# Optimization experiments

Hardware: AMD Instinct MI355X
Metric: run time of the kernel (lower is better)

Reference implementation:

```python
import jax, jax.numpy as jnp
import numpy as np

INV_SQRT2 = 0.7071067811865476
N, E, K, S = 10000, 120000, 8, 7
DE, DA, DT, DR, DC = 128, 128, 64, 16, 16
T = E * K

def act(x):
    return jax.nn.silu(x)

def residual_stack(x, Ws):
    # Ws: (n_layers, 2, D, D); GemNet ResidualLayer: two Dense+act, scaled skip
    for lw in Ws:
        y = act(act(x @ lw[0]) @ lw[1])
        x = (x + y) * INV_SQRT2
    return x

def bilinear(rbf_W1, sph, m, id_reduce, id_ragged, W):
    # EfficientInteractionBilinear (GemNet): ragged scatter into (E,Kmax,emb) then basis contractions
    m2 = jnp.zeros((rbf_W1.shape[0], sph.shape[1], m.shape[-1]), m.dtype)
    m2 = m2.at[id_reduce, id_ragged].set(m)          # (E, K, DT)
    sum_k = jnp.einsum('eks,ekc->esc', sph, m2)      # (E, S, DT)
    a = jnp.einsum('ejs,esc->ejc', rbf_W1, sum_k)    # (E, DC, DT)
    return jnp.einsum('ejc,cju->eu', a, W)           # (E, DT)

def _forward(h, m_st, rbf_h, rbf3, cbf_rbfW1, cbf_sph,
             W_mlp_st, W_m_kt, W_t_rbf, W_down, W_bil, W_st3, W_ts3,
             res_before, res_after, W_ae_rbf, W_ae_in, res_atom, W_asi, res_m,
             idx_s, idx_t, idx_swap, id3_kt, id3_st, id3_ragged_idx):
    x_skip = m_st @ W_mlp_st
    # --- TripletInteraction ---
    m_kt = act(m_st @ W_m_kt)
    m_kt = m_kt * (rbf3 @ W_t_rbf)        # scale_rbf == 1.0 (identity ScaleFactor)
    m_kt = act(m_kt @ W_down)             # (E, DT)
    xb = bilinear(cbf_rbfW1, cbf_sph, m_kt[id3_kt], id3_st, id3_ragged_idx, W_bil)
    x_st = act(xb @ W_st3)
    x_ts = act(xb @ W_ts3)[idx_swap]
    x3 = (x_st + x_ts) * INV_SQRT2
    # --- merge + residual stacks ---
    x = (x_skip + x3) * INV_SQRT2
    x = residual_stack(x, res_before)
    x = (x + m_st) * INV_SQRT2
    x = residual_stack(x, res_after)
    # --- AtomEmbedding: edge->atom scatter-add ---
    xa = x * (rbf_h @ W_ae_rbf)
    h2 = jax.ops.segment_sum(xa, idx_t, num_segments=h.shape[0])  # scale_sum == 1.0
    h_new = residual_stack(act(h2 @ W_ae_in), res_atom)
    # --- AtomSelfInteraction: gather-concat-Dense ---
    m = act(jnp.concatenate([h_new[idx_s], h_new[idx_t], x], axis=-1) @ W_asi)
    m = residual_stack(m, res_m)
    m = (m + x) * INV_SQRT2
    return h_new, m

def setup_inputs():
    key = jax.random.key(0)
    ks = jax.random.split(key, 24)
    def w(k, shape):
        return jax.random.normal(k, shape, jnp.float32) * (1.0 / np.sqrt(shape[-2]))
    return dict(
        h=jax.random.normal(ks[0], (N, DA), jnp.float32),
        m_st=jax.random.normal(ks[1], (E, DE), jnp.float32),
        rbf_h=jax.random.uniform(ks[2], (E, DR), jnp.float32),
        rbf3=jax.random.uniform(ks[3], (E, DR), jnp.float32),
        cbf_rbfW1=jax.random.normal(ks[4], (E, DC, S), jnp.float32) * 0.2,
        cbf_sph=jax.random.normal(ks[5], (E, K, S), jnp.float32) * 0.2,
        W_mlp_st=w(ks[6], (DE, DE)),
        W_m_kt=w(ks[7], (DE, DE)),
        W_t_rbf=w(ks[8], (DR, DE)),
        W_down=w(ks[9], (DE, DT)),
        W_bil=jax.random.normal(ks[10], (DT, DC, DT), jnp.float32) * (1.0 / np.sqrt(DT * DC)),
        W_st3=w(ks[11], (DT, DE)),
        W_ts3=w(ks[12], (DT, DE)),
        res_before=w(ks[13], (1, 2, DE, DE)),
        res_after=w(ks[14], (2, 2, DE, DE)),
        W_ae_rbf=w(ks[15], (DR, DE)),
        W_ae_in=w(ks[16], (DE, DA)),
        res_atom=w(ks[17], (2, 2, DA, DA)),
        W_asi=w(ks[18], (2 * DA + DE, DE)),
        res_m=w(ks[19], (2, 2, DE, DE)),
        idx_s=jax.random.randint(ks[20], (E,), 0, N, jnp.int32),
        idx_t=jax.random.randint(ks[21], (E,), 0, N, jnp.int32),
        idx_swap=jax.random.permutation(ks[22], E).astype(jnp.int32),
        id3_kt=jax.random.randint(ks[23], (T,), 0, E, jnp.int32),
        id3_st=jnp.repeat(jnp.arange(E, dtype=jnp.int32), K),
        id3_ragged_idx=jnp.tile(jnp.arange(K, dtype=jnp.int32), E),
    )

def reference(h, m_st, rbf_h, rbf3, cbf_rbfW1, cbf_sph,
              W_mlp_st, W_m_kt, W_t_rbf, W_down, W_bil, W_st3, W_ts3,
              res_before, res_after, W_ae_rbf, W_ae_in, res_atom, W_asi, res_m,
              idx_s, idx_t, idx_swap, id3_kt, id3_st, id3_ragged_idx):
    return _forward(h, m_st, rbf_h, rbf3, cbf_rbfW1, cbf_sph,
                    W_mlp_st, W_m_kt, W_t_rbf, W_down, W_bil, W_st3, W_ts3,
                    res_before, res_after, W_ae_rbf, W_ae_in, res_atom, W_asi, res_m,
                    idx_s, idx_t, idx_swap, id3_kt, id3_st, id3_ragged_idx)
```

## Files before the change

### kernel.cpp

```cpp
#include <hip/hip_runtime.h>


#define EE 120000
#define NA 10000

constexpr float C_INV = 0.70710678118654752440f;

using f32x4 = __attribute__((ext_vector_type(4))) float;
using f32x2 = __attribute__((ext_vector_type(2))) float;
using s16x8 = __attribute__((ext_vector_type(8))) short;
using s16x4 = __attribute__((ext_vector_type(4))) short;

__device__ __forceinline__ float act_silu(float x) { return x / (1.0f + __expf(-x)); }

__device__ __forceinline__ unsigned short f2bf(float f) {
    unsigned int u = __float_as_uint(f);
    u += 0x7fffu + ((u >> 16) & 1u);
    return (unsigned short)(u >> 16);
}
__device__ __forceinline__ float bf2f(unsigned short h) {
    return __uint_as_float(((unsigned int)h) << 16);
}
__device__ __forceinline__ unsigned int cvtpk(float a, float b) {
    unsigned int r;
    asm("v_cvt_pk_bf16_f32 %0, %1, %2" : "=v"(r) : "v"(a), "v"(b));
    return r;
}

template<int MT, int KQ>
__device__ __forceinline__ void load_w(const unsigned short* __restrict__ W, int KW,
                                       int l, s16x8 (&a)[MT][KQ])
{
    const int fr = l & 15;
    const int k8 = (l >> 4) << 3;
    #pragma unroll
    for (int mt = 0; mt < MT; ++mt)
        #pragma unroll
        for (int kq = 0; kq < KQ; ++kq)
            a[mt][kq] = *(const s16x8*)&W[(size_t)(mt * 16 + fr) * KW + kq * 32 + k8];
}

template<int MT, int NF, int KQ>
__device__ __forceinline__ void gemm_pre(
    const s16x8 (&a)[MT][KQ], const char* ldsB, int RS,
    int rowBase, int l, f32x4 (&acc)[MT][NF])
{
    const int fr = l & 15;
    const int k8 = (l >> 4) << 3;
    #pragma unroll
    for (int kq = 0; kq < KQ; ++kq) {
        s16x8 b[NF];
        #pragma unroll
        for (int nf = 0; nf < NF; ++nf) {
            const int row = rowBase + nf * 16 + fr;
            const int kb  = ((kq * 32 + k8) * 2) ^ ((row & 7) << 4);
            b[nf] = *(const s16x8*)(ldsB + row * RS + kb);
        }
        #pragma unroll
        for (int mt = 0; mt < MT; ++mt)
            #pragma unroll
            for (int nf = 0; nf < NF; ++nf)
                acc[mt][nf] = __builtin_amdgcn_mfma_f32_16x16x32_bf16(
                    a[mt][kq], b[nf], acc[mt][nf], 0, 0, 0);
    }
}

template<int MT, int NF>
__device__ __forceinline__ void zacc(f32x4 (&acc)[MT][NF])
{
    #pragma unroll
    for (int mt = 0; mt < MT; ++mt)
        #pragma unroll
        for (int nf = 0; nf < NF; ++nf)
            acc[mt][nf] = (f32x4){0.f, 0.f, 0.f, 0.f};
}

__device__ __forceinline__ void packA(char* lds, int RS, int row, int outF0, f32x4 v)
{
    uint2 p;
    p.x = cvtpk(v[0], v[1]);
    p.y = cvtpk(v[2], v[3]);
    *(uint2*)(lds + row * RS + ((outF0 * 2) ^ ((row & 7) << 4))) = p;
}

__device__ __forceinline__ void store_bf4(unsigned short* dst, f32x4 v)
{
    uint2 p;
    p.x = cvtpk(v[0], v[1]);
    p.y = cvtpk(v[2], v[3]);
    *(uint2*)dst = p;
}

template<int ROWS>
__device__ __forceinline__ void stage_f32(char* lds, const float* __restrict__ src,
                                          int row0, int M, int tid)
{
    #pragma unroll
    for (int u = 0; u < ROWS * 16 / 512; ++u) {
        const int flat = tid + u * 512;
        const int row  = flat >> 4;
        const int k8   = (flat & 15) << 3;
        const int grow = row0 + row;
        uint4 val = {0u, 0u, 0u, 0u};
        if (grow < M) {
            const float* p = src + (size_t)grow * 128 + k8;
            f32x4 lo = *(const f32x4*)p;
            f32x4 hi = *(const f32x4*)(p + 4);
            val.x = cvtpk(lo[0], lo[1]);
            val.y = cvtpk(lo[2], lo[3]);
            val.z = cvtpk(hi[0], hi[1]);
            val.w = cvtpk(hi[2], hi[3]);
        }
        *(uint4*)(lds + row * 256 + ((k8 * 2) ^ ((row & 7) << 4))) = val;
    }
}

template<bool MSTM, int NF>
__device__ __forceinline__ void res_layer(
    char* A, char* B,
    const unsigned short* W0, const unsigned short* W1,
    int wm, int wn, int l, f32x4 (&x)[2][NF],
    const s16x4 (*ms)[NF])
{
    const int fr = l & 15;
    const int fq = (l >> 4) << 2;

    s16x8 aw[2][4];
    load_w<2, 4>(W0 + (size_t)(wm * 32) * 128, 128, l, aw);
    f32x4 acc[2][NF];
    zacc(acc);
    gemm_pre<2, NF, 4>(aw, A, 256, wn * NF * 16, l, acc);

    s16x8 aw1[2][4];
    load_w<2, 4>(W1 + (size_t)(wm * 32) * 128, 128, l, aw1);

    #pragma unroll
    for (int mt = 0; mt < 2; ++mt)
        #pragma unroll
        for (int nf = 0; nf < NF; ++nf) {
            const int row = wn * NF * 16 + nf * 16 + fr;
            const int of0 = wm * 32 + mt * 16 + fq;
            f32x4 v;
            #pragma unroll
            for (int q = 0; q < 4; ++q) v[q] = act_silu(acc[mt][nf][q]);
            packA(B, 256, row, of0, v);
        }
    __syncthreads();

    zacc(acc);
    gemm_pre<2, NF, 4>(aw1, B, 256, wn * NF * 16, l, acc);
    #pragma unroll
    for (int mt = 0; mt < 2; ++mt)
        #pragma unroll
        for (int nf = 0; nf < NF; ++nf) {
            const int row = wn * NF * 16 + nf * 16 + fr;
            const int of0 = wm * 32 + mt * 16 + fq;
            #pragma unroll
            for (int q = 0; q < 4; ++q)
                x[mt][nf][q] = (x[mt][nf][q] + act_silu(acc[mt][nf][q])) * C_INV;
            if (MSTM) {
                #pragma unroll
                for (int q = 0; q < 4; ++q)
                    x[mt][nf][q] = (x[mt][nf][q] +
                                    bf2f((unsigned short)ms[mt][nf][q])) * C_INV;
            }
            packA(A, 256, row, of0, x[mt][nf]);
        }
    __syncthreads();
}

__device__ __forceinline__ s16x4 read_frag(const char* lds, int row, int of0)
{
    return *(const s16x4*)(lds + row * 256 + ((of0 * 2) ^ ((row & 7) << 4)));
}

__global__ __launch_bounds__(512, 4) void front_k(
    const float* __restrict__ m_st, const unsigned short* __restrict__ scale_b,
    const unsigned short* __restrict__ Wmkt, const unsigned short* __restrict__ Wdown,
    unsigned short* __restrict__ mkt_b)
{
    __shared__ char A[128 * 256];
    const int tid = threadIdx.x;
    const int l = tid & 63, w = tid >> 6, wm = w & 3, wn = w >> 2;
    const int fr = l & 15, fq = (l >> 4) << 2;
    const int row0 = blockIdx.x * 128;

    s16x8 aw[2][4];
    load_w<2, 4>(Wmkt + (size_t)(wm * 32) * 128, 128, l, aw);

    stage_f32<128>(A, m_st, row0, EE, tid);
    __syncthreads();

    f32x4 acc[2][4];
    zacc(acc);
    gemm_pre<2, 4, 4>(aw, A, 256, wn * 64, l, acc);

    s16x8 aw2[1][4];
    load_w<1, 4>(Wdown + (size_t)(wm * 16) * 128, 128, l, aw2);

    __syncthreads();
    #pragma unroll
    for (int mt = 0; mt < 2; ++mt)
        #pragma unroll
        for (int nf = 0; nf < 4; ++nf) {
            const int row = wn * 64 + nf * 16 + fr;
            const int grow = row0 + row;
            const int of0 = wm * 32 + mt * 16 + fq;
            f32x4 v = {0.f, 0.f, 0.f, 0.f};
            if (grow < EE) {
                s16x4 sc = *(const s16x4*)&scale_b[(size_t)grow * 128 + of0];
                #pragma unroll
                for (int q = 0; q < 4; ++q)
                    v[q] = act_silu(acc[mt][nf][q]) * bf2f((unsigned short)sc[q]);
            }
            packA(A, 256, row, of0, v);
        }
    __syncthreads();

    f32x4 acc2[1][4];
    zacc(acc2);
    gemm_pre<1, 4, 4>(aw2, A, 256, wn * 64, l, acc2);
    #pragma unroll
    for (int nf = 0; nf < 4; ++nf) {
        const int row = wn * 64 + nf * 16 + fr;
        const int grow = row0 + row;
        if (grow >= EE) continue;
        const int of0 = wm * 16 + fq;
        f32x4 v;
        #pragma unroll
        for (int q = 0; q < 4; ++q) v[q] = act_silu(acc2[0][nf][q]);
        store_bf4(&mkt_b[(size_t)grow * 64 + of0], v);
    }
}

__global__ __launch_bounds__(512, 4) void st3ts3_k(
    const unsigned short* __restrict__ xb_b,
    const unsigned short* __restrict__ Wst3, const unsigned short* __restrict__ Wts3,
    unsigned short* __restrict__ yst, unsigned short* __restrict__ yts)
{
    __shared__ char A[128 * 128];
    const int tid = threadIdx.x;
    const int l = tid & 63, w = tid >> 6, wm = w & 3, wn = w >> 2;
    const int fr = l & 15, fq = (l >> 4) << 2;
    const int row0 = blockIdx.x * 128;

    s16x8 awS[2][2], awT[2][2];
    load_w<2, 2>(Wst3 + (size_t)(wm * 32) * 64, 64, l, awS);
    load_w<2, 2>(Wts3 + (size_t)(wm * 32) * 64, 64, l, awT);

    #pragma unroll
    for (int u = 0; u < 2; ++u) {
        const int flat = tid + u * 512;
        const int row = flat >> 3;
        const int k8 = (flat & 7) << 3;
        const int grow = row0 + row;
        s16x8 v = {0, 0, 0, 0, 0, 0, 0, 0};
        if (grow < EE) v = *(const s16x8*)&xb_b[(size_t)grow * 64 + k8];
        *(s16x8*)(A + row * 128 + ((k8 * 2) ^ ((row & 7) << 4))) = v;
    }
    __syncthreads();

    f32x4 aS[2][4], aT[2][4];
    zacc(aS); zacc(aT);
    {
        const int k8 = (l >> 4) << 3;
        #pragma unroll
        for (int kq = 0; kq < 2; ++kq) {
            s16x8 b[4];
            #pragma unroll
            for (int nf = 0; nf < 4; ++nf) {
                const int row = wn * 64 + nf * 16 + fr;
                const int kb  = ((kq * 32 + k8) * 2) ^ ((row & 7) << 4);
                b[nf] = *(const s16x8*)(A + row * 128 + kb);
            }
            #pragma unroll
            for (int mt = 0; mt < 2; ++mt)
                #pragma unroll
                for (int nf = 0; nf < 4; ++nf) {
                    aS[mt][nf] = __builtin_amdgcn_mfma_f32_16x16x32_bf16(
                        awS[mt][kq], b[nf], aS[mt][nf], 0, 0, 0);
                    aT[mt][nf] = __builtin_amdgcn_mfma_f32_16x16x32_bf16(
                        awT[mt][kq], b[nf], aT[mt][nf], 0, 0, 0);
                }
        }
    }

    #pragma unroll
    for (int mt = 0; mt < 2; ++mt)
        #pragma unroll
        for (int nf = 0; nf < 4; ++nf) {
            const int row = wn * 64 + nf * 16 + fr;
            const int grow = row0 + row;
            if (grow >= EE) continue;
            const int of0 = wm * 32 + mt * 16 + fq;
            f32x4 vs, vt;
            #pragma unroll
            for (int q = 0; q < 4; ++q) {
                vs[q] = act_silu(aS[mt][nf][q]);
                vt[q] = act_silu(aT[mt][nf][q]);
            }
            store_bf4(&yst[(size_t)grow * 128 + of0], vs);
            store_bf4(&yts[(size_t)grow * 128 + of0], vt);
        }
}

__global__ __launch_bounds__(512, 4) void chain_k(
    const float* __restrict__ m_st,
    const unsigned short* __restrict__ yst, const unsigned short* __restrict__ yts,
    const int* __restrict__ idx_swap,
    const unsigned short* __restrict__ Wmlp,
    const unsigned short* __restrict__ Wrb0, const unsigned short* __restrict__ Wrb1,
    const unsigned short* __restrict__ Wra0, const unsigned short* __restrict__ Wra1,
    const unsigned short* __restrict__ Wra2, const unsigned short* __restrict__ Wra3,
    unsigned short* __restrict__ xb_out)
{
    __shared__ char A[128 * 256];
    __shared__ char B[128 * 256];
    const int tid = threadIdx.x;
    const int l = tid & 63, w = tid >> 6, wm = w & 3, wn = w >> 2;
    const int fr = l & 15, fq = (l >> 4) << 2;
    const int row0 = blockIdx.x * 128;

    s16x8 aw[2][4];
    load_w<2, 4>(Wmlp + (size_t)(wm * 32) * 128, 128, l, aw);

    stage_f32<128>(A, m_st, row0, EE, tid);
    __syncthreads();

    f32x4 acc[2][4];
    zacc(acc);
    gemm_pre<2, 4, 4>(aw, A, 256, wn * 64, l, acc);

    s16x4 ms[2][4];
    #pragma unroll
    for (int mt = 0; mt < 2; ++mt)
        #pragma unroll
        for (int nf = 0; nf < 4; ++nf)
            ms[mt][nf] = read_frag(A, wn * 64 + nf * 16 + fr, wm * 32 + mt * 16 + fq);

    f32x4 x[2][4];
    #pragma unroll
    for (int mt = 0; mt < 2; ++mt)
        #pragma unroll
        for (int nf = 0; nf < 4; ++nf) {
            const int row = wn * 64 + nf * 16 + fr;
            const int grow = row0 + row;
            const int of0 = wm * 32 + mt * 16 + fq;
            if (grow < EE) {
                s16x4 a = *(const s16x4*)&yst[(size_t)grow * 128 + of0];
                const int sw = idx_swap[grow];
                s16x4 b = *(const s16x4*)&yts[(size_t)sw * 128 + of0];
                #pragma unroll
                for (int q = 0; q < 4; ++q)
                    x[mt][nf][q] = (acc[mt][nf][q] +
                        (bf2f((unsigned short)a[q]) + bf2f((unsigned short)b[q])) * C_INV) * C_INV;
            } else {
                x[mt][nf] = (f32x4){0.f, 0.f, 0.f, 0.f};
            }
        }
    __syncthreads();
    #pragma unroll
    for (int mt = 0; mt < 2; ++mt)
        #pragma unroll
        for (int nf = 0; nf < 4; ++nf)
            packA(A, 256, wn * 64 + nf * 16 + fr, wm * 32 + mt * 16 + fq, x[mt][nf]);
    __syncthreads();

    res_layer<true , 4>(A, B, Wrb0, Wrb1, wm, wn, l, x, ms);
    res_layer<false, 4>(A, B, Wra0, Wra1, wm, wn, l, x, nullptr);
    res_layer<false, 4>(A, B, Wra2, Wra3, wm, wn, l, x, nullptr);

    #pragma unroll
    for (int mt = 0; mt < 2; ++mt)
        #pragma unroll
        for (int nf = 0; nf < 4; ++nf) {
            const int row = wn * 64 + nf * 16 + fr;
            const int grow = row0 + row;
            if (grow >= EE) continue;
            const int of0 = wm * 32 + mt * 16 + fq;
            store_bf4(&xb_out[(size_t)grow * 128 + of0], x[mt][nf]);
        }
}

__global__ __launch_bounds__(512, 4) void atom_k(
    const float* __restrict__ h2,
    const unsigned short* __restrict__ Wae,
    const unsigned short* __restrict__ Wr0, const unsigned short* __restrict__ Wr1,
    const unsigned short* __restrict__ Wr2, const unsigned short* __restrict__ Wr3,
    float* __restrict__ out_h, unsigned short* __restrict__ h_b)
{
    __shared__ char A[64 * 256];
    __shared__ char B[64 * 256];
    const int tid = threadIdx.x;
    const int l = tid & 63, w = tid >> 6, wm = w & 3, wn = w >> 2;
    const int fr = l & 15, fq = (l >> 4) << 2;
    const int row0 = blockIdx.x * 64;

    s16x8 aw[2][4];
    load_w<2, 4>(Wae + (size_t)(wm * 32) * 128, 128, l, aw);

    stage_f32<64>(A, h2, row0, NA, tid);
    __syncthreads();

    f32x4 acc[2][2];
    zacc(acc);
    gemm_pre<2, 2, 4>(aw, A, 256, wn * 32, l, acc);
    f32x4 x[2][2];
    #pragma unroll
    for (int mt = 0; mt < 2; ++mt)
        #pragma unroll
        for (int nf = 0; nf < 2; ++nf)
            #pragma unroll
            for (int q = 0; q < 4; ++q)
                x[mt][nf][q] = act_silu(acc[mt][nf][q]);
    __syncthreads();
    #pragma unroll
    for (int mt = 0; mt < 2; ++mt)
        #pragma unroll
        for (int nf = 0; nf < 2; ++nf)
            packA(A, 256, wn * 32 + nf * 16 + fr, wm * 32 + mt * 16 + fq, x[mt][nf]);
    __syncthreads();

    res_layer<false, 2>(A, B, Wr0, Wr1, wm, wn, l, x, nullptr);
    res_layer<false, 2>(A, B, Wr2, Wr3, wm, wn, l, x, nullptr);

    #pragma unroll
    for (int mt = 0; mt < 2; ++mt)
        #pragma unroll
        for (int nf = 0; nf < 2; ++nf) {
            const int row = wn * 32 + nf * 16 + fr;
            const int grow = row0 + row;
            if (grow >= NA) continue;
            const int of0 = wm * 32 + mt * 16 + fq;
            *(f32x4*)&out_h[(size_t)grow * 128 + of0] = x[mt][nf];
            store_bf4(&h_b[(size_t)grow * 128 + of0], x[mt][nf]);
        }
}

__global__ __launch_bounds__(512, 4) void asi_k(
    const unsigned short* __restrict__ h_b, const unsigned short* __restrict__ x_b,
    const int* __restrict__ idx_s, const int* __restrict__ idx_t,
    const unsigned short* __restrict__ Wasi,
    const unsigned short* __restrict__ Wm0, const unsigned short* __restrict__ Wm1,
    const unsigned short* __restrict__ Wm2, const unsigned short* __restrict__ Wm3,
    float* __restrict__ out_m)
{
    __shared__ char A[128 * 256];
    __shared__ char B[128 * 256];
    const int tid = threadIdx.x;
    const int l = tid & 63, w = tid >> 6, wm = w & 3, wn = w >> 2;
    const int fr = l & 15, fq = (l >> 4) << 2;
    const int row0 = blockIdx.x * 128;

    f32x4 acc[2][4];
    zacc(acc);

    for (int c = 0; c < 3; ++c) {
        s16x8 aw[2][4];
        load_w<2, 4>(Wasi + (size_t)(wm * 32) * 384 + c * 128, 384, l, aw);
        #pragma unroll
        for (int u = 0; u < 4; ++u) {
            const int flat = tid + u * 512;
            const int row = flat >> 4;
            const int k8 = (flat & 15) << 3;
            const int grow = row0 + row;
            s16x8 v = {0, 0, 0, 0, 0, 0, 0, 0};
            if (grow < EE) {
                const unsigned short* src =
                    (c == 0) ? h_b + (size_t)idx_s[grow] * 128
                  : (c == 1) ? h_b + (size_t)idx_t[grow] * 128
                             : x_b + (size_t)grow * 128;
                v = *(const s16x8*)&src[k8];
            }
            *(s16x8*)(A + row * 256 + ((k8 * 2) ^ ((row & 7) << 4))) = v;
        }
        __syncthreads();
        gemm_pre<2, 4, 4>(aw, A, 256, wn * 64, l, acc);
        __syncthreads();
    }

    f32x4 x[2][4];
    #pragma unroll
    for (int mt = 0; mt < 2; ++mt)
        #pragma unroll
        for (int nf = 0; nf < 4; ++nf)
            #pragma unroll
            for (int q = 0; q < 4; ++q)
                x[mt][nf][q] = act_silu(acc[mt][nf][q]);
    #pragma unroll
    for (int mt = 0; mt < 2; ++mt)
        #pragma unroll
        for (int nf = 0; nf < 4; ++nf)
            packA(A, 256, wn * 64 + nf * 16 + fr, wm * 32 + mt * 16 + fq, x[mt][nf]);
    __syncthreads();

    res_layer<false, 4>(A, B, Wm0, Wm1, wm, wn, l, x, nullptr);
    res_layer<false, 4>(A, B, Wm2, Wm3, wm, wn, l, x, nullptr);

    #pragma unroll
    for (int mt = 0; mt < 2; ++mt)
        #pragma unroll
        for (int nf = 0; nf < 4; ++nf) {
            const int row = wn * 64 + nf * 16 + fr;
            const int grow = row0 + row;
            if (grow >= EE) continue;
            const int of0 = wm * 32 + mt * 16 + fq;
            s16x4 xv = *(const s16x4*)&x_b[(size_t)grow * 128 + of0];
            f32x4 o;
            #pragma unroll
            for (int q = 0; q < 4; ++q)
                o[q] = (x[mt][nf][q] + bf2f((unsigned short)xv[q])) * C_INV;
            *(f32x4*)&out_m[(size_t)grow * 128 + of0] = o;
        }
}

__global__ __launch_bounds__(256) void rbf_scale_k(
    const float* __restrict__ A, const float* __restrict__ W,
    unsigned short* __restrict__ out, int M)
{
    __shared__ float Ws[16][128];
    const int tid = threadIdx.x;
    #pragma unroll
    for (int t = tid; t < 512; t += 256) {
        int kk = t >> 5, c4 = (t & 31) << 2;
        *(float4*)&Ws[kk][c4] = *(const float4*)(W + kk * 128 + c4);
    }
    __syncthreads();
    const int tx = tid & 31, ty = tid >> 5;
    const int row0 = blockIdx.x * 128;
    #pragma unroll
    for (int i = 0; i < 16; ++i) {
        const int row = row0 + ty + i * 8;
        if (row >= M) continue;
        float av[16];
        #pragma unroll
        for (int j = 0; j < 4; ++j) {
            float4 a = *(const float4*)(A + (size_t)row * 16 + j * 4);
            av[j * 4] = a.x; av[j * 4 + 1] = a.y; av[j * 4 + 2] = a.z; av[j * 4 + 3] = a.w;
        }
        f32x4 s = {0.f, 0.f, 0.f, 0.f};
        #pragma unroll
        for (int k = 0; k < 16; ++k) {
            float4 wv = *(const float4*)&Ws[k][tx * 4];
            s[0] += av[k] * wv.x; s[1] += av[k] * wv.y;
            s[2] += av[k] * wv.z; s[3] += av[k] * wv.w;
        }
        store_bf4(&out[(size_t)row * 128 + tx * 4], s);
    }
}

__global__ void hist_k(const int* __restrict__ idxt, int* __restrict__ cnt)
{
    int i = blockIdx.x * 256 + threadIdx.x;
    if (i < EE) atomicAdd(&cnt[idxt[i]], 1);
}

__global__ __launch_bounds__(256) void scan_k(const int* __restrict__ cnt,
                                              int* __restrict__ start, int* __restrict__ wrk)
{
    __shared__ int ps[256];
    const int t = threadIdx.x;
    int s = 0;
    for (int j = 0; j < 40; ++j) {
        int idx = t * 40 + j;
        if (idx < NA) s += cnt[idx];
    }
    ps[t] = s;
    __syncthreads();
    for (int off = 1; off < 256; off <<= 1) {
        int v = (t >= off) ? ps[t - off] : 0;
        __syncthreads();
        ps[t] += v;
        __syncthreads();
    }
    int run = ps[t] - s;
    for (int j = 0; j < 40; ++j) {
        int idx = t * 40 + j;
        if (idx < NA) {
            start[idx] = run;
            wrk[idx] = run;
            run += cnt[idx];
        }
    }
    if (t == 255) start[NA] = ps[255];
}

__global__ void place_k(const int* __restrict__ idxt, int* __restrict__ wrk,
                        int* __restrict__ order)
{
    int i = blockIdx.x * 256 + threadIdx.x;
    if (i < EE) {
        int pos = atomicAdd(&wrk[idxt[i]], 1);
        order[pos] = i;
    }
}

__global__ __launch_bounds__(256) void segsum_k(
    const unsigned short* __restrict__ x_b, const float* __restrict__ rbf_h,
    const float* __restrict__ Wae, const int* __restrict__ start,
    const int* __restrict__ order, float* __restrict__ h2)
{
    const int tid = threadIdx.x;
    const int l = tid & 63, w = tid >> 6;
    const int a = blockIdx.x * 4 + w;
    if (a >= NA) return;

    float wc[32];
    #pragma unroll
    for (int j = 0; j < 16; ++j) {
        f32x2 v = *(const f32x2*)(Wae + j * 128 + 2 * l);
        wc[2 * j] = v[0]; wc[2 * j + 1] = v[1];
    }

    const int s = start[a], e_end = start[a + 1];
    float acc0 = 0.f, acc1 = 0.f;
    for (int i = s; i < e_end; ++i) {
        const int e = __builtin_amdgcn_readfirstlane(order[i]);
        const unsigned int xv = *(const unsigned int*)(x_b + (size_t)e * 128 + 2 * l);
        const float* rp = rbf_h + (size_t)e * 16;
        float c0 = 0.f, c1 = 0.f;
        #pragma unroll
        for (int j = 0; j < 16; ++j) {
            float r = rp[j];
            c0 += r * wc[2 * j];
            c1 += r * wc[2 * j + 1];
        }
        acc0 += bf2f((unsigned short)(xv & 0xffff)) * c0;
        acc1 += bf2f((unsigned short)(xv >> 16)) * c1;
    }
    f32x2 o; o[0] = acc0; o[1] = acc1;
    *(f32x2*)&h2[(size_t)a * 128 + 2 * l] = o;
}

__global__ void wconv_k(const float* __restrict__ Wbil, unsigned short* __restrict__ WT)
{
    int t = blockIdx.x * 256 + threadIdx.x;
    int u = t >> 10, k = t & 1023, j = k >> 6, c = k & 63;
    WT[t] = f2bf(Wbil[(size_t)(c * 16 + j) * 64 + u]);
}

struct WDesc { const float* src; int K; int N; int off; };
struct WTab  { WDesc d[21]; };

__global__ void wconvall_k(WTab tab, unsigned short* __restrict__ dst)
{
    WDesc d = tab.d[blockIdx.x];
    const int tot = d.K * d.N;
    for (int i = threadIdx.x; i < tot; i += 256) {
        int n = i / d.K, k = i - n * d.K;
        dst[d.off + i] = f2bf(d.src[(size_t)k * d.N + n]);
    }
}

__device__ __forceinline__ float rlc(const f32x4& cv, int idx, int lbase)
{
    const int c = idx & 3;
    float comp = (c == 0) ? cv[0] : (c == 1) ? cv[1] : (c == 2) ? cv[2] : cv[3];
    return __uint_as_float(__builtin_amdgcn_readlane(__float_as_uint(comp),
                                                     lbase + (idx >> 2)));
}

__device__ __forceinline__ void bl_stage(
    const float* __restrict__ sph, const float* __restrict__ rbfW1,
    const int* __restrict__ id3kt, int eG, int l,
    f32x4& cv, int (&ids)[8])
{
    cv = (f32x4){0.f, 0.f, 0.f, 0.f};
    if (l < 14)       cv = *(const f32x4*)(sph   + (size_t)eG * 56  + l * 4);
    else if (l < 42)  cv = *(const f32x4*)(rbfW1 + (size_t)eG * 112 + (l - 14) * 4);
    #pragma unroll
    for (int k = 0; k < 8; ++k) ids[k] = id3kt[eG * 8 + k];
}

__device__ __forceinline__ void bl_gather(
    const unsigned short* __restrict__ mkt, const int (&ids)[8], int l,
    unsigned int (&m2)[8])
{
    #pragma unroll
    for (int k = 0; k < 8; ++k)
        m2[k] = mkt[(size_t)ids[k] * 64 + l];
}

__device__ __forceinline__ void bl_compute(
    const f32x4& cv, const unsigned int (&m2)[8],
    unsigned short* __restrict__ aS, int eL, int l)
{
    float sk[7] = {0.f, 0.f, 0.f, 0.f, 0.f, 0.f, 0.f};
    #pragma unroll
    for (int k = 0; k < 8; ++k) {
        const float mv = __uint_as_float(m2[k] << 16);
        #pragma unroll
        for (int s = 0; s < 7; ++s)
            sk[s] += rlc(cv, k * 7 + s, 0) * mv;
    }
    unsigned short* arow = aS + eL * 1024;
    const int lsw = l ^ ((eL & 7) << 3);
    #pragma unroll
    for (int j = 0; j < 16; ++j) {
        float av = 0.f;
        #pragma unroll
        for (int s = 0; s < 7; ++s)
            av += rlc(cv, j * 7 + s, 14) * sk[s];
        arow[j * 64 + lsw] = f2bf(av);
    }
}

__global__ __launch_bounds__(512) void bilinear6_k(
    const unsigned short* __restrict__ mkt,
    const float* __restrict__ rbfW1,
    const float* __restrict__ sph,
    const int*   __restrict__ id3kt,
    const unsigned short* __restrict__ WT,
    unsigned short* __restrict__ xb)
{
    __shared__ unsigned short aS[32 * 1024];
    float* pS = (float*)aS;

    const int tid = threadIdx.x;
    const int l   = tid & 63;
    const int w   = tid >> 6;
    const int e0  = blockIdx.x * 32;

    s16x8 bfrag[4][4];
    {
        const int u  = l & 15;
        const int kh = w * 128 + ((l >> 4) << 3);
        #pragma unroll
        for (int nt = 0; nt < 4; ++nt)
            #pragma unroll
            for (int kq = 0; kq < 4; ++kq)
                bfrag[nt][kq] = *(const s16x8*)&WT[(size_t)(nt * 16 + u) * 1024 + kh + kq * 32];
    }

    f32x4 cv0, cv1, cv2, cv3;
    int  id0[8], id1[8], id2[8], id3[8];
    unsigned int m0[8], m1[8], m2v[8], m3[8];

    bl_stage(sph, rbfW1, id3kt, e0 + 0 * 8 + w, l, cv0, id0);
    bl_stage(sph, rbfW1, id3kt, e0 + 1 * 8 + w, l, cv1, id1);
    bl_gather(mkt, id0, l, m0);
    bl_gather(mkt, id1, l, m1);
    bl_stage(sph, rbfW1, id3kt, e0 + 2 * 8 + w, l, cv2, id2);
    bl_compute(cv0, m0, aS, 0 * 8 + w, l);
    bl_gather(mkt, id2, l, m2v);
    bl_stage(sph, rbfW1, id3kt, e0 + 3 * 8 + w, l, cv3, id3);
    bl_compute(cv1, m1, aS, 1 * 8 + w, l);
    bl_gather(mkt, id3, l, m3);
    bl_compute(cv2, m2v, aS, 2 * 8 + w, l);
    bl_compute(cv3, m3, aS, 3 * 8 + w, l);
    __syncthreads();

    f32x4 acc[2][4];
    #pragma unroll
    for (int mt = 0; mt < 2; ++mt)
        #pragma unroll
        for (int nt = 0; nt < 4; ++nt)
            acc[mt][nt] = (f32x4){0.f, 0.f, 0.f, 0.f};

    const int kbase = w * 128 + ((l >> 4) << 3);
    #pragma unroll
    for (int kq = 0; kq < 4; ++kq) {
        s16x8 afr[2];
        #pragma unroll
        for (int mt = 0; mt < 2; ++mt) {
            const int row = mt * 16 + (l & 15);
            const int kk  = (kbase + kq * 32) ^ ((row & 7) << 3);
            afr[mt] = *(const s16x8*)&aS[row * 1024 + kk];
        }
        #pragma unroll
        for (int mt = 0; mt < 2; ++mt)
            #pragma unroll
            for (int nt = 0; nt < 4; ++nt)
                acc[mt][nt] = __builtin_amdgcn_mfma_f32_16x16x32_bf16(
                    afr[mt], bfrag[nt][kq], acc[mt][nt], 0, 0, 0);
    }
    __syncthreads();

    #pragma unroll
    for (int mt = 0; mt < 2; ++mt)
        #pragma unroll
        for (int nt = 0; nt < 4; ++nt)
            #pragma unroll
            for (int q = 0; q < 4; ++q) {
                const int e = mt * 16 + ((l >> 4) << 2) + q;
                const int u = nt * 16 + (l & 15);
                pS[(w * 32 + e) * 64 + u] = acc[mt][nt][q];
            }
    __syncthreads();

    {
        const int e  = tid >> 4;
        const int u0 = (tid & 15) << 2;
        f32x4 s = (f32x4){0.f, 0.f, 0.f, 0.f};
        #pragma unroll
        for (int ww = 0; ww < 8; ++ww)
            s += *(const f32x4*)&pS[(ww * 32 + e) * 64 + u0];
        store_bf4(&xb[(size_t)(e0 + e) * 64 + u0], s);
    }
}

extern "C" void kernel_launch(void* const* d_in, const int* in_sizes, int n_in,
                              void* d_out, int out_size, void* d_ws, size_t ws_size,
                              hipStream_t stream)
{
    const float* m_st      = (const float*)d_in[1];
    const float* rbf_h     = (const float*)d_in[2];
    const float* rbf3      = (const float*)d_in[3];
    const float* cbf_rbfW1 = (const float*)d_in[4];
    const float* cbf_sph   = (const float*)d_in[5];
    const float* W_mlp_st  = (const float*)d_in[6];
    const float* W_m_kt    = (const float*)d_in[7];
    const float* W_t_rbf   = (const float*)d_in[8];
    const float* W_down    = (const float*)d_in[9];
    const float* W_bil     = (const float*)d_in[10];
    const float* W_st3     = (const float*)d_in[11];
    const float* W_ts3     = (const float*)d_in[12];
    const float* resb      = (const float*)d_in[13];
    const float* resa      = (const float*)d_in[14];
    const float* W_ae_rbf  = (const float*)d_in[15];
    const float* W_ae_in   = (const float*)d_in[16];
    const float* resat     = (const float*)d_in[17];
    const float* W_asi     = (const float*)d_in[18];
    const float* resm      = (const float*)d_in[19];
    const int*   idx_s     = (const int*)d_in[20];
    const int*   idx_t     = (const int*)d_in[21];
    const int*   idx_swap  = (const int*)d_in[22];
    const int*   id3_kt    = (const int*)d_in[23];

    float* h2 = (float*)d_ws;
    unsigned short* scale_b = (unsigned short*)(h2 + (size_t)NA * 128);
    unsigned short* yst_b   = scale_b;
    unsigned short* yts_b   = scale_b + (size_t)EE * 128;
    unsigned short* x_b     = yts_b + (size_t)EE * 128;
    unsigned short* mkt_b   = x_b + (size_t)EE * 128;
    unsigned short* xb_b    = mkt_b + (size_t)EE * 64;
    unsigned short* h_b     = xb_b + (size_t)EE * 64;
    unsigned short* WTbil   = h_b + (size_t)NA * 128;
    unsigned short* WTall   = WTbil + 65536;
    int* cnt   = (int*)(WTall + 352256);
    int* start = cnt + NA;
    int* wrk   = start + NA + 1;
    int* order = wrk + NA;

    float* out_h = (float*)d_out;
    float* out_m = out_h + (size_t)NA * 128;

    const dim3 blk(256);
    const dim3 blk5(512);
    const int gE  = (EE + 127) / 128;
    const int gN64 = (NA + 63) / 64;
    constexpr size_t SQ = 128 * 128;

    WTab tab; int off = 0; int oi = 0;
    auto put = [&](const float* s, int K, int N) {
        int o = off; tab.d[oi].src = s; tab.d[oi].K = K; tab.d[oi].N = N;
        tab.d[oi].off = o; ++oi; off += K * N; return o;
    };
    const int o_mlp  = put(W_mlp_st, 128, 128);
    const int o_mktw = put(W_m_kt, 128, 128);
    const int o_down = put(W_down, 128, 64);
    const int o_st3  = put(W_st3, 64, 128);
    const int o_ts3  = put(W_ts3, 64, 128);
    const int o_rb0  = put(resb, 128, 128);
    const int o_rb1  = put(resb + SQ, 128, 128);
    const int o_ra0  = put(resa, 128, 128);
    const int o_ra1  = put(resa + SQ, 128, 128);
    const int o_ra2  = put(resa + 2 * SQ, 128, 128);
    const int o_ra3  = put(resa + 3 * SQ, 128, 128);
    const int o_aein = put(W_ae_in, 128, 128);
    const int o_rat0 = put(resat, 128, 128);
    const int o_rat1 = put(resat + SQ, 128, 128);
    const int o_rat2 = put(resat + 2 * SQ, 128, 128);
    const int o_rat3 = put(resat + 3 * SQ, 128, 128);
    const int o_asi  = put(W_asi, 384, 128);
    const int o_rm0  = put(resm, 128, 128);
    const int o_rm1  = put(resm + SQ, 128, 128);
    const int o_rm2  = put(resm + 2 * SQ, 128, 128);
    const int o_rm3  = put(resm + 3 * SQ, 128, 128);

    hipMemsetAsync(cnt, 0, NA * sizeof(int), stream);
    wconv_k<<<65536 / 256, blk, 0, stream>>>(W_bil, WTbil);
    wconvall_k<<<21, blk, 0, stream>>>(tab, WTall);
    hist_k<<<(EE + 255) / 256, blk, 0, stream>>>(idx_t, cnt);
    scan_k<<<1, blk, 0, stream>>>(cnt, start, wrk);
    place_k<<<(EE + 255) / 256, blk, 0, stream>>>(idx_t, wrk, order);

    rbf_scale_k<<<gE, blk, 0, stream>>>(rbf3, W_t_rbf, scale_b, EE);
    front_k<<<gE, blk5, 0, stream>>>(m_st, scale_b, WTall + o_mktw, WTall + o_down, mkt_b);
    bilinear6_k<<<EE / 32, blk5, 0, stream>>>(
        mkt_b, cbf_rbfW1, cbf_sph, id3_kt, WTbil, xb_b);
    st3ts3_k<<<gE, blk5, 0, stream>>>(xb_b, WTall + o_st3, WTall + o_ts3, yst_b, yts_b);
    chain_k<<<gE, blk5, 0, stream>>>(
        m_st, yst_b, yts_b, idx_swap,
        WTall + o_mlp, WTall + o_rb0, WTall + o_rb1,
        WTall + o_ra0, WTall + o_ra1, WTall + o_ra2, WTall + o_ra3,
        x_b);
    segsum_k<<<(NA + 3) / 4, blk, 0, stream>>>(x_b, rbf_h, W_ae_rbf, start, order, h2);
    atom_k<<<gN64, blk5, 0, stream>>>(
        h2, WTall + o_aein,
        WTall + o_rat0, WTall + o_rat1, WTall + o_rat2, WTall + o_rat3,
        out_h, h_b);
    asi_k<<<gE, blk5, 0, stream>>>(
        h_b, x_b, idx_s, idx_t,
        WTall + o_asi,
        WTall + o_rm0, WTall + o_rm1, WTall + o_rm2, WTall + o_rm3,
        out_m);
}
```

Before: 691.0 us.

## Fuse st3/ts3 dense layers into bilinear kernel epilogue

Removes the separate st3ts3 kernel and computes the two 64->128 dense+SiLU projections inside the bilinear kernel. The reduced xb tile is packed to bf16 in swizzled shared memory, and half the waves apply W_st3 while the other half apply W_ts3. This drops the global write and re-read of xb and one kernel launch. In exchange the bilinear kernel needs extra registers for the weight fragments and extra barriers, which may reduce its occupancy.

```diff
diff --git a/kernel.cpp b/kernel.cpp
--- a/kernel.cpp
+++ b/kernel.cpp
@@ -231,77 +231,6 @@
         for (int q = 0; q < 4; ++q) v[q] = act_silu(acc2[0][nf][q]);
         store_bf4(&mkt_b[(size_t)grow * 64 + of0], v);
     }
-}
-
-__global__ __launch_bounds__(512, 4) void st3ts3_k(
-    const unsigned short* __restrict__ xb_b,
-    const unsigned short* __restrict__ Wst3, const unsigned short* __restrict__ Wts3,
-    unsigned short* __restrict__ yst, unsigned short* __restrict__ yts)
-{
-    __shared__ char A[128 * 128];
-    const int tid = threadIdx.x;
-    const int l = tid & 63, w = tid >> 6, wm = w & 3, wn = w >> 2;
-    const int fr = l & 15, fq = (l >> 4) << 2;
-    const int row0 = blockIdx.x * 128;
-
-    s16x8 awS[2][2], awT[2][2];
-    load_w<2, 2>(Wst3 + (size_t)(wm * 32) * 64, 64, l, awS);
-    load_w<2, 2>(Wts3 + (size_t)(wm * 32) * 64, 64, l, awT);
-
-    #pragma unroll
-    for (int u = 0; u < 2; ++u) {
-        const int flat = tid + u * 512;
-        const int row = flat >> 3;
-        const int k8 = (flat & 7) << 3;
-        const int grow = row0 + row;
-        s16x8 v = {0, 0, 0, 0, 0, 0, 0, 0};
-        if (grow < EE) v = *(const s16x8*)&xb_b[(size_t)grow * 64 + k8];
-        *(s16x8*)(A + row * 128 + ((k8 * 2) ^ ((row & 7) << 4))) = v;
-    }
-    __syncthreads();
-
-    f32x4 aS[2][4], aT[2][4];
-    zacc(aS); zacc(aT);
-    {
-        const int k8 = (l >> 4) << 3;
-        #pragma unroll
-        for (int kq = 0; kq < 2; ++kq) {
-            s16x8 b[4];
-            #pragma unroll
-            for (int nf = 0; nf < 4; ++nf) {
-                const int row = wn * 64 + nf * 16 + fr;
-                const int kb  = ((kq * 32 + k8) * 2) ^ ((row & 7) << 4);
-                b[nf] = *(const s16x8*)(A + row * 128 + kb);
-            }
-            #pragma unroll
-            for (int mt = 0; mt < 2; ++mt)
-                #pragma unroll
-                for (int nf = 0; nf < 4; ++nf) {
-                    aS[mt][nf] = __builtin_amdgcn_mfma_f32_16x16x32_bf16(
-                        awS[mt][kq], b[nf], aS[mt][nf], 0, 0, 0);
-                    aT[mt][nf] = __builtin_amdgcn_mfma_f32_16x16x32_bf16(
-                        awT[mt][kq], b[nf], aT[mt][nf], 0, 0, 0);
-                }
-        }
-    }
-
-    #pragma unroll
-    for (int mt = 0; mt < 2; ++mt)
-        #pragma unroll
-        for (int nf = 0; nf < 4; ++nf) {
-            const int row = wn * 64 + nf * 16 + fr;
-            const int grow = row0 + row;
-            if (grow >= EE) continue;
-            const int of0 = wm * 32 + mt * 16 + fq;
-            f32x4 vs, vt;
-            #pragma unroll
-            for (int q = 0; q < 4; ++q) {
-                vs[q] = act_silu(aS[mt][nf][q]);
-                vt[q] = act_silu(aT[mt][nf][q]);
-            }
-            store_bf4(&yst[(size_t)grow * 128 + of0], vs);
-            store_bf4(&yts[(size_t)grow * 128 + of0], vt);
-        }
 }
 
 __global__ __launch_bounds__(512, 4) void chain_k(
@@ -705,13 +634,16 @@
     }
 }
 
-__global__ __launch_bounds__(512) void bilinear6_k(
+__global__ __launch_bounds__(512) void bilinear7_k(
     const unsigned short* __restrict__ mkt,
     const float* __restrict__ rbfW1,
     const float* __restrict__ sph,
     const int*   __restrict__ id3kt,
     const unsigned short* __restrict__ WT,
-    unsigned short* __restrict__ xb)
+    const unsigned short* __restrict__ Wst3,
+    const unsigned short* __restrict__ Wts3,
+    unsigned short* __restrict__ yst,
+    unsigned short* __restrict__ yts)
 {
     __shared__ unsigned short aS[32 * 1024];
     float* pS = (float*)aS;
@@ -720,6 +652,8 @@
     const int l   = tid & 63;
     const int w   = tid >> 6;
     const int e0  = blockIdx.x * 32;
+    const int fr  = l & 15;
+    const int fq  = (l >> 4) << 2;
 
     s16x8 bfrag[4][4];
     {
@@ -788,15 +722,49 @@
             }
     __syncthreads();
 
+    f32x4 s;
     {
         const int e  = tid >> 4;
         const int u0 = (tid & 15) << 2;
-        f32x4 s = (f32x4){0.f, 0.f, 0.f, 0.f};
+        s = (f32x4){0.f, 0.f, 0.f, 0.f};
         #pragma unroll
         for (int ww = 0; ww < 8; ++ww)
             s += *(const f32x4*)&pS[(ww * 32 + e) * 64 + u0];
-        store_bf4(&xb[(size_t)(e0 + e) * 64 + u0], s);
-    }
+    }
+    __syncthreads();
+
+    unsigned short* xbS = aS;
+    {
+        const int e  = tid >> 4;
+        const int u0 = (tid & 15) << 2;
+        uint2 p;
+        p.x = cvtpk(s[0], s[1]);
+        p.y = cvtpk(s[2], s[3]);
+        *(uint2*)((char*)xbS + e * 128 + ((u0 * 2) ^ ((e & 7) << 4))) = p;
+    }
+    __syncthreads();
+
+    const unsigned short* Wsel = (w < 4) ? Wst3 : Wts3;
+    unsigned short*       ysel = (w < 4) ? yst : yts;
+    const int wmF = w & 3;
+
+    s16x8 awF[2][2];
+    load_w<2, 2>(Wsel + (size_t)(wmF * 32) * 64, 64, l, awF);
+    f32x4 accF[2][2];
+    zacc(accF);
+    gemm_pre<2, 2, 2>(awF, (const char*)xbS, 128, 0, l, accF);
+
+    #pragma unroll
+    for (int mt = 0; mt < 2; ++mt)
+        #pragma unroll
+        for (int nf = 0; nf < 2; ++nf) {
+            const int row = nf * 16 + fr;
+            const int of0 = wmF * 32 + mt * 16 + fq;
+            f32x4 v;
+            #pragma unroll
+            for (int q = 0; q < 4; ++q) v[q] = act_silu(accF[mt][nf][q]);
+            store_bf4(&ysel[(size_t)(e0 + row) * 128 + of0], v);
+        }
 }
 
 extern "C" void kernel_launch(void* const* d_in, const int* in_sizes, int n_in,
@@ -887,9 +855,9 @@
 
     rbf_scale_k<<<gE, blk, 0, stream>>>(rbf3, W_t_rbf, scale_b, EE);
     front_k<<<gE, blk5, 0, stream>>>(m_st, scale_b, WTall + o_mktw, WTall + o_down, mkt_b);
-    bilinear6_k<<<EE / 32, blk5, 0, stream>>>(
-        mkt_b, cbf_rbfW1, cbf_sph, id3_kt, WTbil, xb_b);
-    st3ts3_k<<<gE, blk5, 0, stream>>>(xb_b, WTall + o_st3, WTall + o_ts3, yst_b, yts_b);
+    bilinear7_k<<<EE / 32, blk5, 0, stream>>>(
+        mkt_b, cbf_rbfW1, cbf_sph, id3_kt, WTbil,
+        WTall + o_st3, WTall + o_ts3, yst_b, yts_b);
     chain_k<<<gE, blk5, 0, stream>>>(
         m_st, yst_b, yts_b, idx_swap,
         WTall + o_mlp, WTall + o_rb0, WTall + o_rb1,
```

New measurement: 669.0 us. 1.03x faster.
